# Optimization experiments

Hardware: AMD Instinct MI355X
Metric: run time of the kernel (lower is better)

## Reference

```python
import jax, jax.numpy as jnp
import numpy as np

B, H, W, C = 2, 64, 64, 256
NH, K = 8, 7
HD = C // NH


def setup_inputs() -> dict:
    key = jax.random.key(0)
    ks = jax.random.split(key, 5)
    s = lambda fan: 1.0 / np.sqrt(fan)
    return {
        "x": jax.random.normal(ks[0], (B, H, W, C), jnp.float32),
        "ln1_w": jnp.ones((C,), jnp.float32),
        "ln1_b": jnp.zeros((C,), jnp.float32),
        "qkv_w": jax.random.normal(ks[1], (3 * C, C), jnp.float32) * s(C),
        "qkv_b": jnp.zeros((3 * C,), jnp.float32),
        "proj_w": jax.random.normal(ks[2], (C, C), jnp.float32) * s(C),
        "proj_b": jnp.zeros((C,), jnp.float32),
        "ln2_w": jnp.ones((C,), jnp.float32),
        "ln2_b": jnp.zeros((C,), jnp.float32),
        "fc1_w": jax.random.normal(ks[3], (4 * C, C), jnp.float32) * s(C),
        "fc1_b": jnp.zeros((4 * C,), jnp.float32),
        "fc2_w": jax.random.normal(ks[4], (C, 4 * C), jnp.float32) * s(4 * C),
        "fc2_b": jnp.zeros((C,), jnp.float32),
    }


def _ln(x, w, b, eps=1e-5):
    m = x.mean(-1, keepdims=True)
    v = ((x - m) ** 2).mean(-1, keepdims=True)
    return (x - m) * jax.lax.rsqrt(v + eps) * w + b


def _nbr_idx(n, k):
    # NATTEN non-causal window: start clamped so the full k-window fits in [0, n)
    half = k // 2
    start = np.clip(np.arange(n) - half, 0, n - k)
    return jnp.asarray(start[:, None] + np.arange(k)[None, :])  # [n, k]


def reference(x, ln1_w, ln1_b, qkv_w, qkv_b, proj_w, proj_b,
              ln2_w, ln2_b, fc1_w, fc1_b, fc2_w, fc2_b):
    shortcut = x
    xn = _ln(x, ln1_w, ln1_b)
    qkv = (xn @ qkv_w.T + qkv_b).reshape(B, H, W, 3, NH, HD)
    qkv = jnp.transpose(qkv, (3, 0, 4, 1, 2, 5))  # [3,B,NH,H,W,HD]
    q, k, v = qkv[0], qkv[1], qkv[2]
    q = q * (HD ** -0.5)
    ih = _nbr_idx(H, K)[:, None, :, None]   # [H,1,K,1]
    iw = _nbr_idx(W, K)[None, :, None, :]   # [1,W,1,K]
    # gather 7x7 neighborhoods -> [B,NH,H,W,K,K,HD] -> [B,NH,H,W,K*K,HD]
    k_nb = k[:, :, ih, iw, :].reshape(B, NH, H, W, K * K, HD)
    v_nb = v[:, :, ih, iw, :].reshape(B, NH, H, W, K * K, HD)
    attn = jnp.einsum("bnijd,bnijkd->bnijk", q, k_nb)  # na2d_qk
    attn = jax.nn.softmax(attn, axis=-1)
    out = jnp.einsum("bnijk,bnijkd->bnijd", attn, v_nb)  # na2d_av
    out = jnp.transpose(out, (0, 2, 3, 1, 4)).reshape(B, H, W, C)
    out = out @ proj_w.T + proj_b
    x = shortcut + out
    h = _ln(x, ln2_w, ln2_b)
    h = jax.nn.gelu(h @ fc1_w.T + fc1_b, approximate=False)
    h = h @ fc2_w.T + fc2_b
    return x + h
```

## Files before the change

kernel.cpp:

```cpp
#include <hip/hip_runtime.h>
#include <math.h>

#define Hdim 64
#define Wdim 64
#define Cc 256
#define NHh 8
#define NTOK 8192

typedef unsigned short ushortT;
typedef __attribute__((ext_vector_type(8))) short short8;
typedef __attribute__((ext_vector_type(4))) float floatx4;

__device__ inline ushortT f2bf(float x) {
    union { float f; unsigned u; } v; v.f = x;
    unsigned r = (v.u + 0x7fffu + ((v.u >> 16) & 1u)) >> 16;
    return (ushortT)r;
}

#define GLOAD_LDS16(g, l) __builtin_amdgcn_global_load_lds( \
    (const __attribute__((address_space(1))) unsigned int*)(g), \
    (__attribute__((address_space(3))) unsigned int*)(l), 16, 0, 0)

__global__ __launch_bounds__(256) void convert_weights(
        const float* __restrict__ qkv_w, const float* __restrict__ proj_w,
        const float* __restrict__ fc1_w, const float* __restrict__ fc2_w,
        ushortT* __restrict__ o_qkv, ushortT* __restrict__ o_proj,
        ushortT* __restrict__ o_fc1, ushortT* __restrict__ o_fc2) {
    int idx = blockIdx.x * 256 + threadIdx.x;
    const float* src; ushortT* dst; int local;
    if (idx < 49152)        { src = qkv_w;  dst = o_qkv;  local = idx; }
    else if (idx < 65536)   { src = proj_w; dst = o_proj; local = idx - 49152; }
    else if (idx < 131072)  { src = fc1_w;  dst = o_fc1;  local = idx - 65536; }
    else                    { src = fc2_w;  dst = o_fc2;  local = idx - 131072; }
    float4 v = ((const float4*)src)[local];
    ushortT o[4] = {f2bf(v.x), f2bf(v.y), f2bf(v.z), f2bf(v.w)};
    *(uint2*)(dst + (size_t)local * 4) = *(uint2*)o;
}

__global__ __launch_bounds__(256) void ln_bf16(const float* __restrict__ x,
                                               const float* __restrict__ w,
                                               const float* __restrict__ b,
                                               ushortT* __restrict__ y) {
    int t = blockIdx.x;
    int c = threadIdx.x;
    float v = x[(size_t)t * Cc + c];
    float s = v, sq = v * v;
#pragma unroll
    for (int off = 32; off > 0; off >>= 1) {
        s  += __shfl_xor(s, off, 64);
        sq += __shfl_xor(sq, off, 64);
    }
    __shared__ float sh[8];
    int wave = threadIdx.x >> 6, lane = threadIdx.x & 63;
    if (lane == 0) { sh[wave] = s; sh[4 + wave] = sq; }
    __syncthreads();
    float sum = sh[0] + sh[1] + sh[2] + sh[3];
    float ssq = sh[4] + sh[5] + sh[6] + sh[7];
    float mean = sum * (1.0f / Cc);
    float var  = ssq * (1.0f / Cc) - mean * mean;
    float r = rsqrtf(var + 1e-5f);
    y[(size_t)t * Cc + c] = f2bf((v - mean) * r * w[c] + b[c]);
}

template <int EPI, bool OUTBF>
__global__ __launch_bounds__(256) void gemm_bf16_v2(const ushortT* __restrict__ A,
                                                    const ushortT* __restrict__ Bw,
                                                    const float* __restrict__ bias,
                                                    const float* __restrict__ res,
                                                    void* __restrict__ Cout,
                                                    int N, int K) {
    __shared__ ushortT As[64 * 64];
    __shared__ ushortT Bs[64 * 64];
    const int tid  = threadIdx.x;
    const int wave = tid >> 6, lane = tid & 63;
    const int wm = wave >> 1, wn = wave & 1;
    const int ln16 = lane & 15, kg = lane >> 4;
    const int m0 = blockIdx.y * 64, n0 = blockIdx.x * 64;
    const int g8 = (((lane & 7) ^ (lane >> 3)) * 8);
    const int srow = wave * 16 + (lane >> 3);

    const floatx4 fzero = {0.f, 0.f, 0.f, 0.f};
    floatx4 acc[2][2];
#pragma unroll
    for (int i = 0; i < 2; ++i)
#pragma unroll
        for (int j = 0; j < 2; ++j) acc[i][j] = fzero;

    for (int kt = 0; kt < K; kt += 64) {
#pragma unroll
        for (int p = 0; p < 2; ++p) {
            int row = srow + p * 8;
            GLOAD_LDS16(A  + (size_t)(m0 + row) * K + kt + g8, As + wave * 1024 + p * 512);
            GLOAD_LDS16(Bw + (size_t)(n0 + row) * K + kt + g8, Bs + wave * 1024 + p * 512);
        }
        __syncthreads();
#pragma unroll
        for (int s = 0; s < 2; ++s) {
            short8 a[2], b[2];
#pragma unroll
            for (int i = 0; i < 2; ++i) {
                int ra = wm * 32 + i * 16 + ln16;
                a[i] = *(const short8*)(As + ra * 64 + (((s * 4 + kg) ^ (ln16 & 7)) * 8));
            }
#pragma unroll
            for (int j = 0; j < 2; ++j) {
                int rb = wn * 32 + j * 16 + ln16;
                b[j] = *(const short8*)(Bs + rb * 64 + (((s * 4 + kg) ^ (ln16 & 7)) * 8));
            }
#pragma unroll
            for (int i = 0; i < 2; ++i)
#pragma unroll
                for (int j = 0; j < 2; ++j)
                    acc[i][j] = __builtin_amdgcn_mfma_f32_16x16x32_bf16(a[i], b[j], acc[i][j], 0, 0, 0);
        }
        __syncthreads();
    }

#pragma unroll
    for (int i = 0; i < 2; ++i) {
#pragma unroll
        for (int r = 0; r < 4; ++r) {
            int row = m0 + wm * 32 + i * 16 + kg * 4 + r;
#pragma unroll
            for (int j = 0; j < 2; ++j) {
                int col = n0 + wn * 32 + j * 16 + ln16;
                float v = acc[i][j][r] + bias[col];
                if (EPI == 1) v += res[(size_t)row * N + col];
                if (EPI == 2) v = 0.5f * v * (1.0f + erff(v * 0.70710678118654752f));
                if (OUTBF) ((ushortT*)Cout)[(size_t)row * N + col] = f2bf(v);
                else       ((float*)Cout)[(size_t)row * N + col]  = v;
            }
        }
    }
}

__global__ __launch_bounds__(256) void natten_v2(const float* __restrict__ qkv,
                                                 ushortT* __restrict__ attn_out) {
    __shared__ float Ks[196][36];
    __shared__ float Ps[64][50];
    const int tid = threadIdx.x;
    const int bid = blockIdx.x;
    const int tile = bid & 63;
    const int h = (bid >> 6) & 7;
    const int b = bid >> 9;
    const int ti = tile >> 3, tj = tile & 7;
    const int r0 = min(max(ti * 8 - 3, 0), Hdim - 14);
    const int c0 = min(max(tj * 8 - 3, 0), Wdim - 14);

    for (int idx = tid; idx < 196 * 8; idx += 256) {
        int pos = idx >> 3, q4 = idx & 7;
        int dr = pos / 14, dc = pos % 14;
        size_t tok = (size_t)((b * Hdim + r0 + dr) * Wdim + (c0 + dc));
        *(float4*)&Ks[pos][q4 * 4] = *(const float4*)(qkv + tok * 768 + 256 + h * 32 + q4 * 4);
    }
    __syncthreads();

    const int tl = tid >> 2, s = tid & 3;
    const int i = ti * 8 + (tl >> 3), j = tj * 8 + (tl & 7);
    const int si = min(max(i - 3, 0), Hdim - 7), sj = min(max(j - 3, 0), Wdim - 7);
    const int lr = si - r0, lc = sj - c0;
    const size_t tq = (size_t)((b * Hdim + i) * Wdim + j);

    float q[32];
    {
        const float4* qp = (const float4*)(qkv + tq * 768 + h * 32);
#pragma unroll
        for (int d4 = 0; d4 < 8; ++d4) {
            float4 qv = qp[d4];
            q[d4 * 4 + 0] = qv.x * 0.17677669529663687f;
            q[d4 * 4 + 1] = qv.y * 0.17677669529663687f;
            q[d4 * 4 + 2] = qv.z * 0.17677669529663687f;
            q[d4 * 4 + 3] = qv.w * 0.17677669529663687f;
        }
    }

    float sc[13];
    int cnt = 0;
    for (int n = s; n < 49; n += 4) {
        int di = n / 7, dj = n - di * 7;
        const float* kr = &Ks[(lr + di) * 14 + (lc + dj)][0];
        float a = 0.f;
#pragma unroll
        for (int d4 = 0; d4 < 8; ++d4) {
            float4 kv = *(const float4*)(kr + d4 * 4);
            a += q[d4*4+0]*kv.x + q[d4*4+1]*kv.y + q[d4*4+2]*kv.z + q[d4*4+3]*kv.w;
        }
        sc[cnt++] = a;
    }
    float m = -1e30f;
    for (int c = 0; c < cnt; ++c) m = fmaxf(m, sc[c]);
    m = fmaxf(m, __shfl_xor(m, 1, 64));
    m = fmaxf(m, __shfl_xor(m, 2, 64));
    float tot = 0.f;
    for (int c = 0; c < cnt; ++c) { sc[c] = __expf(sc[c] - m); tot += sc[c]; }
    tot += __shfl_xor(tot, 1, 64);
    tot += __shfl_xor(tot, 2, 64);
    float inv = 1.0f / tot;
    cnt = 0;
    for (int n = s; n < 49; n += 4) Ps[tl][n] = sc[cnt++] * inv;
    __syncthreads();

    float o[8];
#pragma unroll
    for (int d = 0; d < 8; ++d) o[d] = 0.f;
    for (int di = 0; di < 7; ++di) {
        int row = si + di;
#pragma unroll
        for (int dj = 0; dj < 7; ++dj) {
            float p = Ps[tl][di * 7 + dj];
            size_t tokv = (size_t)((b * Hdim + row) * Wdim + (sj + dj));
            const float4* vp = (const float4*)(qkv + tokv * 768 + 512 + h * 32 + s * 8);
            float4 v0 = vp[0], v1 = vp[1];
            o[0] += p * v0.x; o[1] += p * v0.y; o[2] += p * v0.z; o[3] += p * v0.w;
            o[4] += p * v1.x; o[5] += p * v1.y; o[6] += p * v1.z; o[7] += p * v1.w;
        }
    }
    unsigned u[4];
#pragma unroll
    for (int d = 0; d < 4; ++d)
        u[d] = (unsigned)f2bf(o[2 * d]) | ((unsigned)f2bf(o[2 * d + 1]) << 16);
    *(uint4*)(attn_out + tq * 256 + h * 32 + s * 8) = make_uint4(u[0], u[1], u[2], u[3]);
}

extern "C" void kernel_launch(void* const* d_in, const int* in_sizes, int n_in,
                              void* d_out, int out_size, void* d_ws, size_t ws_size,
                              hipStream_t stream) {
    const float* x      = (const float*)d_in[0];
    const float* ln1_w  = (const float*)d_in[1];
    const float* ln1_b  = (const float*)d_in[2];
    const float* qkv_w  = (const float*)d_in[3];
    const float* qkv_b  = (const float*)d_in[4];
    const float* proj_w = (const float*)d_in[5];
    const float* proj_b = (const float*)d_in[6];
    const float* ln2_w  = (const float*)d_in[7];
    const float* ln2_b  = (const float*)d_in[8];
    const float* fc1_w  = (const float*)d_in[9];
    const float* fc1_b  = (const float*)d_in[10];
    const float* fc2_w  = (const float*)d_in[11];
    const float* fc2_b  = (const float*)d_in[12];
    float* out = (float*)d_out;

    char* ws = (char*)d_ws;
    size_t off = 0;
    ushortT* wqkv = (ushortT*)(ws + off); off += (size_t)196608 * 2;
    ushortT* wproj= (ushortT*)(ws + off); off += (size_t)65536 * 2;
    ushortT* wfc1 = (ushortT*)(ws + off); off += (size_t)262144 * 2;
    ushortT* wfc2 = (ushortT*)(ws + off); off += (size_t)262144 * 2;
    ushortT* xn   = (ushortT*)(ws + off); off += (size_t)NTOK * 256 * 2;
    float*   qkvb = (float*)  (ws + off); off += (size_t)NTOK * 768 * 4;
    ushortT* attn = (ushortT*)(ws + off); off += (size_t)NTOK * 256 * 2;
    float*   x2   = (float*)  (ws + off); off += (size_t)NTOK * 256 * 4;
    ushortT* hb   = (ushortT*)(ws + off); off += (size_t)NTOK * 256 * 2;
    ushortT* h1   = (ushortT*)(ws + off); off += (size_t)NTOK * 1024 * 2;

    dim3 blk(256);
    convert_weights<<<768, blk, 0, stream>>>(qkv_w, proj_w, fc1_w, fc2_w,
                                             wqkv, wproj, wfc1, wfc2);
    ln_bf16<<<NTOK, blk, 0, stream>>>(x, ln1_w, ln1_b, xn);
    gemm_bf16_v2<0, false><<<dim3(12, 128), blk, 0, stream>>>(xn, wqkv, qkv_b, nullptr, qkvb, 768, 256);
    natten_v2<<<1024, blk, 0, stream>>>(qkvb, attn);
    gemm_bf16_v2<1, false><<<dim3(4, 128), blk, 0, stream>>>(attn, wproj, proj_b, x, x2, 256, 256);
    ln_bf16<<<NTOK, blk, 0, stream>>>(x2, ln2_w, ln2_b, hb);
    gemm_bf16_v2<2, true><<<dim3(16, 128), blk, 0, stream>>>(hb, wfc1, fc1_b, nullptr, h1, 1024, 256);
    gemm_bf16_v2<1, false><<<dim3(4, 128), blk, 0, stream>>>(h1, wfc2, fc2_b, x2, out, 256, 1024);
}
```

Measured before the change: 169.3 us.

## Rewrite pipeline: bf16 head-major QKV, LDS-staged K/V attention, specialized GEMMs

```diff
diff --git a/kernel.cpp b/kernel.cpp
--- a/kernel.cpp
+++ b/kernel.cpp
@@ -3,8 +3,6 @@
 
 #define Hdim 64
 #define Wdim 64
-#define Cc 256
-#define NHh 8
 #define NTOK 8192
 
 typedef unsigned short ushortT;
@@ -15,6 +13,10 @@
     union { float f; unsigned u; } v; v.f = x;
     unsigned r = (v.u + 0x7fffu + ((v.u >> 16) & 1u)) >> 16;
     return (ushortT)r;
+}
+__device__ inline float bf2f(ushortT u) {
+    union { unsigned u; float f; } v; v.u = ((unsigned)u) << 16;
+    return v.f;
 }
 
 #define GLOAD_LDS16(g, l) __builtin_amdgcn_global_load_lds( \
@@ -37,47 +39,54 @@
     *(uint2*)(dst + (size_t)local * 4) = *(uint2*)o;
 }
 
-__global__ __launch_bounds__(256) void ln_bf16(const float* __restrict__ x,
-                                               const float* __restrict__ w,
-                                               const float* __restrict__ b,
-                                               ushortT* __restrict__ y) {
-    int t = blockIdx.x;
-    int c = threadIdx.x;
-    float v = x[(size_t)t * Cc + c];
-    float s = v, sq = v * v;
+__global__ __launch_bounds__(256) void ln_v2(const float* __restrict__ x,
+                                             const float* __restrict__ w,
+                                             const float* __restrict__ b,
+                                             ushortT* __restrict__ y) {
+    int wave = threadIdx.x >> 6, lane = threadIdx.x & 63;
+    int t = blockIdx.x * 4 + wave;
+    float4 v = *(const float4*)(x + (size_t)t * 256 + lane * 4);
+    float s = v.x + v.y + v.z + v.w;
+    float sq = v.x * v.x + v.y * v.y + v.z * v.z + v.w * v.w;
 #pragma unroll
     for (int off = 32; off > 0; off >>= 1) {
         s  += __shfl_xor(s, off, 64);
         sq += __shfl_xor(sq, off, 64);
     }
-    __shared__ float sh[8];
-    int wave = threadIdx.x >> 6, lane = threadIdx.x & 63;
-    if (lane == 0) { sh[wave] = s; sh[4 + wave] = sq; }
-    __syncthreads();
-    float sum = sh[0] + sh[1] + sh[2] + sh[3];
-    float ssq = sh[4] + sh[5] + sh[6] + sh[7];
-    float mean = sum * (1.0f / Cc);
-    float var  = ssq * (1.0f / Cc) - mean * mean;
+    float mean = s * (1.0f / 256.0f);
+    float var  = sq * (1.0f / 256.0f) - mean * mean;
     float r = rsqrtf(var + 1e-5f);
-    y[(size_t)t * Cc + c] = f2bf((v - mean) * r * w[c] + b[c]);
-}
-
-template <int EPI, bool OUTBF>
-__global__ __launch_bounds__(256) void gemm_bf16_v2(const ushortT* __restrict__ A,
+    float4 wv = *(const float4*)(w + lane * 4);
+    float4 bv = *(const float4*)(b + lane * 4);
+    ushortT o[4] = {f2bf((v.x - mean) * r * wv.x + bv.x),
+                    f2bf((v.y - mean) * r * wv.y + bv.y),
+                    f2bf((v.z - mean) * r * wv.z + bv.z),
+                    f2bf((v.w - mean) * r * wv.w + bv.w)};
+    *(uint2*)(y + (size_t)t * 256 + lane * 4) = *(uint2*)o;
+}
+
+template <int EPI>
+__global__ __launch_bounds__(256, 3) void gemm_k256(const ushortT* __restrict__ A,
                                                     const ushortT* __restrict__ Bw,
                                                     const float* __restrict__ bias,
                                                     const float* __restrict__ res,
-                                                    void* __restrict__ Cout,
-                                                    int N, int K) {
-    __shared__ ushortT As[64 * 64];
-    __shared__ ushortT Bs[64 * 64];
-    const int tid  = threadIdx.x;
-    const int wave = tid >> 6, lane = tid & 63;
+                                                    void* __restrict__ out0,
+                                                    ushortT* __restrict__ kb,
+                                                    ushortT* __restrict__ vb,
+                                                    int N) {
+    __shared__ ushortT As[64 * 256];
+    const int tid = threadIdx.x, wave = tid >> 6, lane = tid & 63;
     const int wm = wave >> 1, wn = wave & 1;
     const int ln16 = lane & 15, kg = lane >> 4;
     const int m0 = blockIdx.y * 64, n0 = blockIdx.x * 64;
-    const int g8 = (((lane & 7) ^ (lane >> 3)) * 8);
-    const int srow = wave * 16 + (lane >> 3);
+
+#pragma unroll
+    for (int rnd = 0; rnd < 8; ++rnd) {
+        int qb = rnd * 256 + wave * 64;
+        int qq = qb + lane;
+        int r = qq >> 5, c = (qq & 31) ^ (r & 7);
+        GLOAD_LDS16(A + (size_t)(m0 + r) * 256 + c * 8, As + qb * 8);
+    }
 
     const floatx4 fzero = {0.f, 0.f, 0.f, 0.f};
     floatx4 acc[2][2];
@@ -86,140 +95,218 @@
 #pragma unroll
         for (int j = 0; j < 2; ++j) acc[i][j] = fzero;
 
-    for (int kt = 0; kt < K; kt += 64) {
-#pragma unroll
-        for (int p = 0; p < 2; ++p) {
-            int row = srow + p * 8;
-            GLOAD_LDS16(A  + (size_t)(m0 + row) * K + kt + g8, As + wave * 1024 + p * 512);
-            GLOAD_LDS16(Bw + (size_t)(n0 + row) * K + kt + g8, Bs + wave * 1024 + p * 512);
+    const ushortT* Brow = Bw + (size_t)(n0 + wn * 32 + ln16) * 256;
+    __syncthreads();
+
+#pragma unroll
+    for (int kk = 0; kk < 8; ++kk) {
+        int c0 = kk * 4 + kg;
+        short8 b0 = *(const short8*)(Brow + kk * 32 + kg * 8);
+        short8 b1 = *(const short8*)(Brow + 16 * 256 + kk * 32 + kg * 8);
+        int ra0 = wm * 32 + ln16;
+        int ra1 = ra0 + 16;
+        short8 a0 = *(const short8*)(As + ra0 * 256 + (c0 ^ (ra0 & 7)) * 8);
+        short8 a1 = *(const short8*)(As + ra1 * 256 + (c0 ^ (ra1 & 7)) * 8);
+        acc[0][0] = __builtin_amdgcn_mfma_f32_16x16x32_bf16(a0, b0, acc[0][0], 0, 0, 0);
+        acc[0][1] = __builtin_amdgcn_mfma_f32_16x16x32_bf16(a0, b1, acc[0][1], 0, 0, 0);
+        acc[1][0] = __builtin_amdgcn_mfma_f32_16x16x32_bf16(a1, b0, acc[1][0], 0, 0, 0);
+        acc[1][1] = __builtin_amdgcn_mfma_f32_16x16x32_bf16(a1, b1, acc[1][1], 0, 0, 0);
+    }
+
+#pragma unroll
+    for (int j = 0; j < 2; ++j) {
+        int col = n0 + wn * 32 + j * 16 + ln16;
+        float bsv = bias[col];
+        if (EPI == 0) {
+            int part = col >> 8, h = (col >> 5) & 7, d = col & 31;
+            ushortT* dst = part == 0 ? (ushortT*)out0 : (part == 1 ? kb : vb);
+            float scl = part == 0 ? 0.17677669529663687f : 1.0f;
+#pragma unroll
+            for (int i = 0; i < 2; ++i)
+#pragma unroll
+                for (int r = 0; r < 4; ++r) {
+                    int row = m0 + wm * 32 + i * 16 + kg * 4 + r;
+                    int bI = row >> 12, tin = row & 4095;
+                    dst[((size_t)(bI * 8 + h) * 4096 + tin) * 32 + d] =
+                        f2bf((acc[i][j][r] + bsv) * scl);
+                }
+        } else {
+#pragma unroll
+            for (int i = 0; i < 2; ++i)
+#pragma unroll
+                for (int r = 0; r < 4; ++r) {
+                    int row = m0 + wm * 32 + i * 16 + kg * 4 + r;
+                    float v = acc[i][j][r] + bsv;
+                    if (EPI == 1) {
+                        v += res[(size_t)row * N + col];
+                        ((float*)out0)[(size_t)row * N + col] = v;
+                    } else {
+                        v = 0.5f * v * (1.0f + erff(v * 0.70710678118654752f));
+                        ((ushortT*)out0)[(size_t)row * N + col] = f2bf(v);
+                    }
+                }
+        }
+    }
+}
+
+__global__ __launch_bounds__(256, 3) void gemm_fc2(const ushortT* __restrict__ A,
+                                                   const ushortT* __restrict__ Bw,
+                                                   const float* __restrict__ bias,
+                                                   const float* __restrict__ res,
+                                                   float* __restrict__ out) {
+    __shared__ ushortT As[32 * 256];
+    const int tid = threadIdx.x, wave = tid >> 6, lane = tid & 63;
+    const int wm = wave >> 1, wn = wave & 1;
+    const int ln16 = lane & 15, kg = lane >> 4;
+    const int m0 = blockIdx.y * 32, n0 = blockIdx.x * 64;
+
+    const floatx4 fzero = {0.f, 0.f, 0.f, 0.f};
+    floatx4 acc[2] = {fzero, fzero};
+    const ushortT* Brow = Bw + (size_t)(n0 + wn * 32 + ln16) * 1024;
+
+    for (int kc = 0; kc < 4; ++kc) {
+#pragma unroll
+        for (int rnd = 0; rnd < 4; ++rnd) {
+            int qb = rnd * 256 + wave * 64;
+            int qq = qb + lane;
+            int r = qq >> 5, c = (qq & 31) ^ (r & 7);
+            GLOAD_LDS16(A + (size_t)(m0 + r) * 1024 + kc * 256 + c * 8, As + qb * 8);
         }
         __syncthreads();
 #pragma unroll
-        for (int s = 0; s < 2; ++s) {
-            short8 a[2], b[2];
-#pragma unroll
-            for (int i = 0; i < 2; ++i) {
-                int ra = wm * 32 + i * 16 + ln16;
-                a[i] = *(const short8*)(As + ra * 64 + (((s * 4 + kg) ^ (ln16 & 7)) * 8));
-            }
-#pragma unroll
-            for (int j = 0; j < 2; ++j) {
-                int rb = wn * 32 + j * 16 + ln16;
-                b[j] = *(const short8*)(Bs + rb * 64 + (((s * 4 + kg) ^ (ln16 & 7)) * 8));
-            }
-#pragma unroll
-            for (int i = 0; i < 2; ++i)
-#pragma unroll
-                for (int j = 0; j < 2; ++j)
-                    acc[i][j] = __builtin_amdgcn_mfma_f32_16x16x32_bf16(a[i], b[j], acc[i][j], 0, 0, 0);
+        for (int kk = 0; kk < 8; ++kk) {
+            int c0 = kk * 4 + kg;
+            int ra = wm * 16 + ln16;
+            short8 a  = *(const short8*)(As + ra * 256 + (c0 ^ (ra & 7)) * 8);
+            short8 b0 = *(const short8*)(Brow + kc * 256 + kk * 32 + kg * 8);
+            short8 b1 = *(const short8*)(Brow + 16 * 1024 + kc * 256 + kk * 32 + kg * 8);
+            acc[0] = __builtin_amdgcn_mfma_f32_16x16x32_bf16(a, b0, acc[0], 0, 0, 0);
+            acc[1] = __builtin_amdgcn_mfma_f32_16x16x32_bf16(a, b1, acc[1], 0, 0, 0);
         }
         __syncthreads();
     }
 
 #pragma unroll
-    for (int i = 0; i < 2; ++i) {
+    for (int j = 0; j < 2; ++j) {
+        int col = n0 + wn * 32 + j * 16 + ln16;
+        float bsv = bias[col];
 #pragma unroll
         for (int r = 0; r < 4; ++r) {
-            int row = m0 + wm * 32 + i * 16 + kg * 4 + r;
-#pragma unroll
-            for (int j = 0; j < 2; ++j) {
-                int col = n0 + wn * 32 + j * 16 + ln16;
-                float v = acc[i][j][r] + bias[col];
-                if (EPI == 1) v += res[(size_t)row * N + col];
-                if (EPI == 2) v = 0.5f * v * (1.0f + erff(v * 0.70710678118654752f));
-                if (OUTBF) ((ushortT*)Cout)[(size_t)row * N + col] = f2bf(v);
-                else       ((float*)Cout)[(size_t)row * N + col]  = v;
-            }
-        }
-    }
-}
-
-__global__ __launch_bounds__(256) void natten_v2(const float* __restrict__ qkv,
+            int row = m0 + wm * 16 + kg * 4 + r;
+            float v = acc[j][r] + bsv + res[(size_t)row * 256 + col];
+            out[(size_t)row * 256 + col] = v;
+        }
+    }
+}
+
+__global__ __launch_bounds__(256) void natten_v3(const ushortT* __restrict__ qb,
+                                                 const ushortT* __restrict__ kb,
+                                                 const ushortT* __restrict__ vb,
                                                  ushortT* __restrict__ attn_out) {
-    __shared__ float Ks[196][36];
-    __shared__ float Ps[64][50];
-    const int tid = threadIdx.x;
-    const int bid = blockIdx.x;
-    const int tile = bid & 63;
-    const int h = (bid >> 6) & 7;
-    const int b = bid >> 9;
+    __shared__ ushortT KVs[2 * 196 * 40];
+    __shared__ float Ps[64][52];
+    ushortT* Ks = KVs;
+    ushortT* Vs = KVs + 196 * 40;
+    const int tid = threadIdx.x, bid = blockIdx.x;
+    const int tile = bid & 63, h = (bid >> 6) & 7, b = bid >> 9;
     const int ti = tile >> 3, tj = tile & 7;
     const int r0 = min(max(ti * 8 - 3, 0), Hdim - 14);
     const int c0 = min(max(tj * 8 - 3, 0), Wdim - 14);
-
-    for (int idx = tid; idx < 196 * 8; idx += 256) {
-        int pos = idx >> 3, q4 = idx & 7;
-        int dr = pos / 14, dc = pos % 14;
-        size_t tok = (size_t)((b * Hdim + r0 + dr) * Wdim + (c0 + dc));
-        *(float4*)&Ks[pos][q4 * 4] = *(const float4*)(qkv + tok * 768 + 256 + h * 32 + q4 * 4);
-    }
-    __syncthreads();
+    const size_t base = (size_t)(b * 8 + h) * 4096 * 32;
+
+    for (int idx = tid; idx < 1568; idx += 256) {
+        int t = idx;
+        const ushortT* src = kb;
+        ushortT* dst = Ks;
+        if (t >= 784) { t -= 784; src = vb; dst = Vs; }
+        int pos = t >> 2, ch = t & 3;
+        int dr = pos / 14, dc = pos - dr * 14;
+        int tok = (r0 + dr) * 64 + (c0 + dc);
+        *(uint4*)(dst + pos * 40 + ch * 8) = *(const uint4*)(src + base + (size_t)tok * 32 + ch * 8);
+    }
 
     const int tl = tid >> 2, s = tid & 3;
     const int i = ti * 8 + (tl >> 3), j = tj * 8 + (tl & 7);
     const int si = min(max(i - 3, 0), Hdim - 7), sj = min(max(j - 3, 0), Wdim - 7);
-    const int lr = si - r0, lc = sj - c0;
-    const size_t tq = (size_t)((b * Hdim + i) * Wdim + j);
+    const int lbase = (si - r0) * 14 + (sj - c0);
+    const int tin = i * 64 + j;
 
     float q[32];
     {
-        const float4* qp = (const float4*)(qkv + tq * 768 + h * 32);
-#pragma unroll
-        for (int d4 = 0; d4 < 8; ++d4) {
-            float4 qv = qp[d4];
-            q[d4 * 4 + 0] = qv.x * 0.17677669529663687f;
-            q[d4 * 4 + 1] = qv.y * 0.17677669529663687f;
-            q[d4 * 4 + 2] = qv.z * 0.17677669529663687f;
-            q[d4 * 4 + 3] = qv.w * 0.17677669529663687f;
-        }
-    }
+        const ushortT* qp = qb + base + (size_t)tin * 32;
+#pragma unroll
+        for (int c4 = 0; c4 < 4; ++c4) {
+            uint4 u = *(const uint4*)(qp + c4 * 8);
+            unsigned uu[4] = {u.x, u.y, u.z, u.w};
+#pragma unroll
+            for (int e = 0; e < 4; ++e) {
+                union { unsigned v; float f; } lo, hi;
+                lo.v = uu[e] << 16; hi.v = uu[e] & 0xffff0000u;
+                q[c4 * 8 + e * 2] = lo.f; q[c4 * 8 + e * 2 + 1] = hi.f;
+            }
+        }
+    }
+    __syncthreads();
 
     float sc[13];
-    int cnt = 0;
-    for (int n = s; n < 49; n += 4) {
-        int di = n / 7, dj = n - di * 7;
-        const float* kr = &Ks[(lr + di) * 14 + (lc + dj)][0];
-        float a = 0.f;
-#pragma unroll
-        for (int d4 = 0; d4 < 8; ++d4) {
-            float4 kv = *(const float4*)(kr + d4 * 4);
-            a += q[d4*4+0]*kv.x + q[d4*4+1]*kv.y + q[d4*4+2]*kv.z + q[d4*4+3]*kv.w;
-        }
-        sc[cnt++] = a;
+#pragma unroll
+    for (int cI = 0; cI < 13; ++cI) {
+        int n = s + cI * 4;
+        if (n < 49) {
+            int di = n / 7, dj = n - di * 7;
+            const ushortT* kr = Ks + (lbase + di * 14 + dj) * 40;
+            float a = 0.f;
+#pragma unroll
+            for (int c4 = 0; c4 < 4; ++c4) {
+                uint4 u = *(const uint4*)(kr + c4 * 8);
+                unsigned uu[4] = {u.x, u.y, u.z, u.w};
+#pragma unroll
+                for (int e = 0; e < 4; ++e) {
+                    union { unsigned v; float f; } lo, hi;
+                    lo.v = uu[e] << 16; hi.v = uu[e] & 0xffff0000u;
+                    a += q[c4 * 8 + e * 2] * lo.f + q[c4 * 8 + e * 2 + 1] * hi.f;
+                }
+            }
+            sc[cI] = a;
+        }
     }
     float m = -1e30f;
-    for (int c = 0; c < cnt; ++c) m = fmaxf(m, sc[c]);
+#pragma unroll
+    for (int cI = 0; cI < 13; ++cI) if (s + cI * 4 < 49) m = fmaxf(m, sc[cI]);
     m = fmaxf(m, __shfl_xor(m, 1, 64));
     m = fmaxf(m, __shfl_xor(m, 2, 64));
     float tot = 0.f;
-    for (int c = 0; c < cnt; ++c) { sc[c] = __expf(sc[c] - m); tot += sc[c]; }
+#pragma unroll
+    for (int cI = 0; cI < 13; ++cI) if (s + cI * 4 < 49) { sc[cI] = __expf(sc[cI] - m); tot += sc[cI]; }
     tot += __shfl_xor(tot, 1, 64);
     tot += __shfl_xor(tot, 2, 64);
     float inv = 1.0f / tot;
-    cnt = 0;
-    for (int n = s; n < 49; n += 4) Ps[tl][n] = sc[cnt++] * inv;
+#pragma unroll
+    for (int cI = 0; cI < 13; ++cI) if (s + cI * 4 < 49) Ps[tl][s + cI * 4] = sc[cI] * inv;
     __syncthreads();
 
-    float o[8];
-#pragma unroll
-    for (int d = 0; d < 8; ++d) o[d] = 0.f;
-    for (int di = 0; di < 7; ++di) {
-        int row = si + di;
-#pragma unroll
-        for (int dj = 0; dj < 7; ++dj) {
-            float p = Ps[tl][di * 7 + dj];
-            size_t tokv = (size_t)((b * Hdim + row) * Wdim + (sj + dj));
-            const float4* vp = (const float4*)(qkv + tokv * 768 + 512 + h * 32 + s * 8);
-            float4 v0 = vp[0], v1 = vp[1];
-            o[0] += p * v0.x; o[1] += p * v0.y; o[2] += p * v0.z; o[3] += p * v0.w;
-            o[4] += p * v1.x; o[5] += p * v1.y; o[6] += p * v1.z; o[7] += p * v1.w;
-        }
-    }
-    unsigned u[4];
+    float o[8] = {0.f, 0.f, 0.f, 0.f, 0.f, 0.f, 0.f, 0.f};
+#pragma unroll
+    for (int n = 0; n < 49; ++n) {
+        int di = n / 7, dj = n - di * 7;
+        float p = Ps[tl][n];
+        const ushortT* vr = Vs + (lbase + di * 14 + dj) * 40 + s * 8;
+        uint4 u = *(const uint4*)vr;
+        unsigned uu[4] = {u.x, u.y, u.z, u.w};
+#pragma unroll
+        for (int e = 0; e < 4; ++e) {
+            union { unsigned v; float f; } lo, hi;
+            lo.v = uu[e] << 16; hi.v = uu[e] & 0xffff0000u;
+            o[e * 2]     += p * lo.f;
+            o[e * 2 + 1] += p * hi.f;
+        }
+    }
+    unsigned up[4];
 #pragma unroll
     for (int d = 0; d < 4; ++d)
-        u[d] = (unsigned)f2bf(o[2 * d]) | ((unsigned)f2bf(o[2 * d + 1]) << 16);
-    *(uint4*)(attn_out + tq * 256 + h * 32 + s * 8) = make_uint4(u[0], u[1], u[2], u[3]);
+        up[d] = (unsigned)f2bf(o[2 * d]) | ((unsigned)f2bf(o[2 * d + 1]) << 16);
+    size_t tq = (size_t)(b * 4096 + tin);
+    *(uint4*)(attn_out + tq * 256 + h * 32 + s * 8) = make_uint4(up[0], up[1], up[2], up[3]);
 }
 
 extern "C" void kernel_launch(void* const* d_in, const int* in_sizes, int n_in,
@@ -247,7 +334,9 @@
     ushortT* wfc1 = (ushortT*)(ws + off); off += (size_t)262144 * 2;
     ushortT* wfc2 = (ushortT*)(ws + off); off += (size_t)262144 * 2;
     ushortT* xn   = (ushortT*)(ws + off); off += (size_t)NTOK * 256 * 2;
-    float*   qkvb = (float*)  (ws + off); off += (size_t)NTOK * 768 * 4;
+    ushortT* qbuf = (ushortT*)(ws + off); off += (size_t)NTOK * 256 * 2;
+    ushortT* kbuf = (ushortT*)(ws + off); off += (size_t)NTOK * 256 * 2;
+    ushortT* vbuf = (ushortT*)(ws + off); off += (size_t)NTOK * 256 * 2;
     ushortT* attn = (ushortT*)(ws + off); off += (size_t)NTOK * 256 * 2;
     float*   x2   = (float*)  (ws + off); off += (size_t)NTOK * 256 * 4;
     ushortT* hb   = (ushortT*)(ws + off); off += (size_t)NTOK * 256 * 2;
@@ -256,11 +345,14 @@
     dim3 blk(256);
     convert_weights<<<768, blk, 0, stream>>>(qkv_w, proj_w, fc1_w, fc2_w,
                                              wqkv, wproj, wfc1, wfc2);
-    ln_bf16<<<NTOK, blk, 0, stream>>>(x, ln1_w, ln1_b, xn);
-    gemm_bf16_v2<0, false><<<dim3(12, 128), blk, 0, stream>>>(xn, wqkv, qkv_b, nullptr, qkvb, 768, 256);
-    natten_v2<<<1024, blk, 0, stream>>>(qkvb, attn);
-    gemm_bf16_v2<1, false><<<dim3(4, 128), blk, 0, stream>>>(attn, wproj, proj_b, x, x2, 256, 256);
-    ln_bf16<<<NTOK, blk, 0, stream>>>(x2, ln2_w, ln2_b, hb);
-    gemm_bf16_v2<2, true><<<dim3(16, 128), blk, 0, stream>>>(hb, wfc1, fc1_b, nullptr, h1, 1024, 256);
-    gemm_bf16_v2<1, false><<<dim3(4, 128), blk, 0, stream>>>(h1, wfc2, fc2_b, x2, out, 256, 1024);
-}
+    ln_v2<<<2048, blk, 0, stream>>>(x, ln1_w, ln1_b, xn);
+    gemm_k256<0><<<dim3(12, 128), blk, 0, stream>>>(xn, wqkv, qkv_b, nullptr,
+                                                    qbuf, kbuf, vbuf, 768);
+    natten_v3<<<1024, blk, 0, stream>>>(qbuf, kbuf, vbuf, attn);
+    gemm_k256<1><<<dim3(4, 128), blk, 0, stream>>>(attn, wproj, proj_b, x,
+                                                   x2, nullptr, nullptr, 256);
+    ln_v2<<<2048, blk, 0, stream>>>(x2, ln2_w, ln2_b, hb);
+    gemm_k256<2><<<dim3(16, 128), blk, 0, stream>>>(hb, wfc1, fc1_b, nullptr,
+                                                    h1, nullptr, nullptr, 1024);
+    gemm_fc2<<<dim3(4, 256), blk, 0, stream>>>(h1, wfc2, fc2_b, x2, out);
+}
```

New measurement: 200.3 us. 1.18x slower.
